# Optimization experiments

Measured on AMD Instinct MI355X. Metric: run time of the kernel, lower is better.

Reference implementation:

```python
import jax, jax.numpy as jnp
import numpy as np

VOCAB, EMB, HID, LAT = 32000, 512, 1024, 512
B, T = 32, 128


def setup_inputs() -> dict:
    key = jax.random.key(0)
    ks = jax.random.split(key, 10)
    s = 0.02
    return {
        "latent_vector": jax.random.normal(ks[0], (B, LAT), jnp.float32),
        "target_tokens": jax.random.randint(ks[1], (B, T), 0, VOCAB),
        "emb": jax.random.normal(ks[2], (VOCAB, EMB), jnp.float32) * s,
        "W_lh": jax.random.normal(ks[3], (HID, LAT), jnp.float32) * s,
        "b_lh": jnp.zeros((HID,), jnp.float32),
        "W_ih": jax.random.normal(ks[4], (4 * HID, EMB), jnp.float32) * s,
        "b_ih": jnp.zeros((4 * HID,), jnp.float32),
        "W_hh": jax.random.normal(ks[5], (4 * HID, HID), jnp.float32) * s,
        "b_hh": jnp.zeros((4 * HID,), jnp.float32),
        "W_out": jax.random.normal(ks[6], (VOCAB, HID), jnp.float32) * s,
        "b_out": jnp.zeros((VOCAB,), jnp.float32),
    }


def reference(latent_vector, target_tokens, emb, W_lh, b_lh, W_ih, b_ih, W_hh, b_hh, W_out, b_out):
    # teacher_forcing_ratio = 1.0 (deterministic): input at step t is target_tokens[:, t-1]
    h = latent_vector @ W_lh.T + b_lh            # [B, HID]
    c = jnp.zeros_like(h)
    xs = emb[target_tokens[:, :-1]]              # [B, T-1, EMB]
    xs = jnp.swapaxes(xs, 0, 1)                  # [T-1, B, EMB]

    def step(carry, x):
        h, c = carry
        gates = x @ W_ih.T + b_ih + h @ W_hh.T + b_hh   # [B, 4*HID]
        i, f, g, o = jnp.split(gates, 4, axis=-1)       # PyTorch LSTM gate order
        c = jax.nn.sigmoid(f) * c + jax.nn.sigmoid(i) * jnp.tanh(g)
        h = jax.nn.sigmoid(o) * jnp.tanh(c)
        logits = h @ W_out.T + b_out                    # [B, VOCAB]
        return (h, c), logits

    _, logits = jax.lax.scan(step, (h, c), xs)          # [T-1, B, VOCAB]
    return jnp.swapaxes(logits, 0, 1)                   # [B, T-1, VOCAB]
```

## Files before the change

kernel.cpp:

```cpp
#include <hip/hip_runtime.h>
#include <cstdint>

typedef __bf16 bf16x8 __attribute__((ext_vector_type(8)));
typedef __bf16 bf16x4 __attribute__((ext_vector_type(4)));
typedef float  f32x4  __attribute__((ext_vector_type(4)));

#define VOCAB 32000
#define EMB   512
#define HID   1024
#define LAT   512
#define BATCH 32
#define TSTEP 127
#define MROWS 4064
#define MPAD  4096
#define G4    4096
#define NBLK  128
#define FSTRIDE 64

__device__ __forceinline__ float sigf(float x){ return 1.0f / (1.0f + __expf(-x)); }
__device__ __forceinline__ float tanhfast(float x){
    float ax = fabsf(x);
    float e  = __expf(-2.0f * ax);
    float t  = (1.0f - e) / (1.0f + e);
    return copysignf(t, x);
}

__device__ __forceinline__ void gll16(void* lds, const void* gsrc){
    __builtin_amdgcn_global_load_lds(
        (const __attribute__((address_space(1))) unsigned int*)gsrc,
        (__attribute__((address_space(3))) unsigned int*)lds,
        16, 0, 0);
}

__global__ __launch_bounds__(256) void cvt_kernel(
    const float* __restrict__ in, __bf16* __restrict__ out, int n4)
{
    int i = blockIdx.x * 256 + threadIdx.x;
    if (i < n4){
        float4 v = ((const float4*)in)[i];
        bf16x4 o = { (__bf16)v.x, (__bf16)v.y, (__bf16)v.z, (__bf16)v.w };
        ((bf16x4*)out)[i] = o;
    }
}

__global__ __launch_bounds__(256) void init_kernel(
    const float* __restrict__ latent,
    const float* __restrict__ Wlh,
    const float* __restrict__ blh,
    __bf16* __restrict__ h0,
    __bf16* __restrict__ Hall,
    unsigned* __restrict__ flags)
{
    if (blockIdx.x == 0 && threadIdx.x < NBLK)
        flags[threadIdx.x * FSTRIDE] = 0u;

    int id = blockIdx.x * 256 + threadIdx.x;
    int b = id >> 10, j = id & 1023;
    float s = blh[j];
    const float4* lr = (const float4*)(latent + (size_t)b * LAT);
    const float4* wr = (const float4*)(Wlh + (size_t)j * LAT);
    for (int k = 0; k < LAT / 4; ++k){
        float4 a = lr[k], w = wr[k];
        s += a.x * w.x + a.y * w.y + a.z * w.z + a.w * w.w;
    }
    h0[id] = (__bf16)s;
    Hall[(size_t)MROWS * HID + id] = (__bf16)0.0f;
}

__global__ __launch_bounds__(256) void gemm_xg(
    const float* __restrict__ emb,
    const float* __restrict__ Wih,
    const int*   __restrict__ tok,
    float*       __restrict__ xg,
    const float* __restrict__ bih,
    const float* __restrict__ bhh)
{
    __shared__ __bf16 As[2][128 * 32];
    __shared__ __bf16 Bs[2][128 * 32];

    const int tid  = threadIdx.x;
    const int wid  = tid >> 6, lane = tid & 63;
    const int tile_n = blockIdx.x, tile_m = blockIdx.y;
    const int wr = wid >> 1, wc = wid & 1;

    f32x4 acc[4][4] = {};

    auto stage = [&](int kt, int buf){
        #pragma unroll
        for (int j = 0; j < 2; ++j){
            const int slot = tid + j * 256;
            const int row  = slot >> 2;
            const int kb   = kt * 32 + (slot & 3) * 8;
            {
                const int brow = tile_n * 128 + row;
                const float4* p = (const float4*)(Wih + (size_t)brow * EMB + kb);
                float4 u = p[0], v = p[1];
                bf16x8 w = { (__bf16)u.x, (__bf16)u.y, (__bf16)u.z, (__bf16)u.w,
                             (__bf16)v.x, (__bf16)v.y, (__bf16)v.z, (__bf16)v.w };
                *(bf16x8*)&Bs[buf][row * 32 + (slot & 3) * 8] = w;
            }
            {
                int r = tile_m * 128 + row;
                int rc = (r < MROWS) ? r : (MROWS - 1);
                int token = tok[(rc & 31) * 128 + (rc >> 5)];
                const float4* p = (const float4*)(emb + (size_t)token * EMB + kb);
                float4 u = p[0], v = p[1];
                bf16x8 w = { (__bf16)u.x, (__bf16)u.y, (__bf16)u.z, (__bf16)u.w,
                             (__bf16)v.x, (__bf16)v.y, (__bf16)v.z, (__bf16)v.w };
                *(bf16x8*)&As[buf][row * 32 + (slot & 3) * 8] = w;
            }
        }
    };

    const int KT = EMB / 32;
    stage(0, 0);
    for (int kt = 0; kt < KT; ++kt){
        const int buf = kt & 1;
        __syncthreads();
        if (kt + 1 < KT) stage(kt + 1, buf ^ 1);
        const __bf16* Abuf = As[buf];
        const __bf16* Bbuf = Bs[buf];
        const int ar = lane & 15, ko = (lane >> 4) * 8;
        bf16x8 av[4], bv[4];
        #pragma unroll
        for (int m = 0; m < 4; ++m)
            av[m] = *(const bf16x8*)&Abuf[(wr * 64 + m * 16 + ar) * 32 + ko];
        #pragma unroll
        for (int n = 0; n < 4; ++n)
            bv[n] = *(const bf16x8*)&Bbuf[(wc * 64 + n * 16 + ar) * 32 + ko];
        #pragma unroll
        for (int m = 0; m < 4; ++m)
            #pragma unroll
            for (int n = 0; n < 4; ++n)
                acc[m][n] = __builtin_amdgcn_mfma_f32_16x16x32_bf16(av[m], bv[n], acc[m][n], 0, 0, 0);
    }

    const int r0 = tile_m * 128 + wr * 64 + ((lane >> 4) << 2);
    const int c0 = tile_n * 128 + wc * 64 + (lane & 15);
    #pragma unroll
    for (int m = 0; m < 4; ++m){
        #pragma unroll
        for (int n = 0; n < 4; ++n){
            const int col = c0 + n * 16;
            float badd = bih[col] + bhh[col];
            #pragma unroll
            for (int q = 0; q < 4; ++q){
                int row = r0 + m * 16 + q;
                xg[(size_t)row * G4 + col] = acc[m][n][q] + badd;
            }
        }
    }
}

#define NTM 32
#define NTN 250
template<int BF16B>
__global__ __launch_bounds__(256) void gemm_logits(
    const __bf16* __restrict__ A,
    const float*  __restrict__ Bf,
    const __bf16* __restrict__ Bb,
    float*        __restrict__ C,
    const float*  __restrict__ bias)
{
    __shared__ __bf16 As[2][128 * 32];
    __shared__ __bf16 Bs[2][128 * 32];

    const int tid  = threadIdx.x;
    const int wid  = tid >> 6, lane = tid & 63;

    const int bid = blockIdx.x;
    const int s   = (bid & 7) * (NTM * NTN / 8) + (bid >> 3);
    const int g   = s / (8 * NTN), rem = s % (8 * NTN);
    const int tile_m = g * 8 + (rem & 7);
    const int tile_n = rem >> 3;

    const int wr = wid >> 1, wc = wid & 1;

    f32x4 acc[4][4] = {};

    auto stage = [&](int kt, int buf){
        const int kb = kt * 32 + (lane & 3) * 8;
        #pragma unroll
        for (int c2 = 0; c2 < 2; ++c2){
            int rA = tile_m * 128 + c2 * 64 + wid * 16 + (lane >> 2);
            gll16(&As[buf][c2 * 2048 + wid * 512], A + (size_t)rA * HID + kb);
            if constexpr (BF16B){
                int rB = tile_n * 128 + c2 * 64 + wid * 16 + (lane >> 2);
                gll16(&Bs[buf][c2 * 2048 + wid * 512], Bb + (size_t)rB * HID + kb);
            }
        }
        if constexpr (!BF16B){
            #pragma unroll
            for (int j = 0; j < 2; ++j){
                const int slot = tid + j * 256;
                const int row  = slot >> 2;
                const int kb2  = kt * 32 + (slot & 3) * 8;
                const int brow = tile_n * 128 + row;
                const float4* p = (const float4*)(Bf + (size_t)brow * HID + kb2);
                float4 u = p[0], v = p[1];
                bf16x8 w = { (__bf16)u.x, (__bf16)u.y, (__bf16)u.z, (__bf16)u.w,
                             (__bf16)v.x, (__bf16)v.y, (__bf16)v.z, (__bf16)v.w };
                *(bf16x8*)&Bs[buf][row * 32 + (slot & 3) * 8] = w;
            }
        }
    };

    const int KT = HID / 32;
    stage(0, 0);
    for (int kt = 0; kt < KT; ++kt){
        const int buf = kt & 1;
        __syncthreads();
        if (kt + 1 < KT) stage(kt + 1, buf ^ 1);
        const __bf16* Abuf = As[buf];
        const __bf16* Bbuf = Bs[buf];
        const int ar = lane & 15, ko = (lane >> 4) * 8;
        bf16x8 av[4], bv[4];
        #pragma unroll
        for (int m = 0; m < 4; ++m)
            av[m] = *(const bf16x8*)&Abuf[(wr * 64 + m * 16 + ar) * 32 + ko];
        #pragma unroll
        for (int n = 0; n < 4; ++n)
            bv[n] = *(const bf16x8*)&Bbuf[(wc * 64 + n * 16 + ar) * 32 + ko];
        #pragma unroll
        for (int m = 0; m < 4; ++m)
            #pragma unroll
            for (int n = 0; n < 4; ++n)
                acc[m][n] = __builtin_amdgcn_mfma_f32_16x16x32_bf16(av[m], bv[n], acc[m][n], 0, 0, 0);
    }

    const int r0 = tile_m * 128 + wr * 64 + ((lane >> 4) << 2);
    const int c0 = tile_n * 128 + wc * 64 + (lane & 15);
    #pragma unroll
    for (int m = 0; m < 4; ++m){
        #pragma unroll
        for (int n = 0; n < 4; ++n){
            const int col = c0 + n * 16;
            float badd = bias[col];
            #pragma unroll
            for (int q = 0; q < 4; ++q){
                int row = r0 + m * 16 + q;
                if (row < MROWS){
                    int t = row >> 5, b = row & 31;
                    __builtin_nontemporal_store(acc[m][n][q] + badd,
                        &C[((size_t)b * TSTEP + t) * VOCAB + col]);
                }
            }
        }
    }
}

__global__ __launch_bounds__(256) void lstm_coop(
    const float*  __restrict__ xg,
    __bf16*       __restrict__ Hall,
    __bf16*       __restrict__ hbuf,
    const __bf16* __restrict__ Whhb,
    unsigned*     __restrict__ flags,
    const float*  __restrict__ Woutf,
    __bf16*       __restrict__ Woutb)
{
    if (blockIdx.x >= NBLK){
        if (Woutb){
            const int n4 = VOCAB * HID / 4;
            int i = (blockIdx.x - NBLK) * 256 + threadIdx.x;
            for (; i < n4; i += NBLK * 256){
                float4 v = ((const float4*)Woutf)[i];
                bf16x4 o = { (__bf16)v.x, (__bf16)v.y, (__bf16)v.z, (__bf16)v.w };
                ((bf16x4*)Woutb)[i] = o;
            }
        }
        return;
    }

    __shared__ float lds_g[4 * 4 * 4 * 64];
    const int tid = threadIdx.x, wid = tid >> 6, lane = tid & 63;
    const int jb = blockIdx.x * 8;

    bf16x8 bfrag[2][8];
    {
        const int gl = lane & 15, ko = (lane >> 4) * 8;
        #pragma unroll
        for (int nt = 0; nt < 2; ++nt){
            int gg = nt * 16 + gl;
            const __bf16* base =
                Whhb + (size_t)((gg >> 3) * HID + jb + (gg & 7)) * HID + wid * 256 + ko;
            #pragma unroll
            for (int ks = 0; ks < 8; ++ks)
                bfrag[nt][ks] = *(const bf16x8*)(base + ks * 32);
        }
    }

    const int b2 = tid >> 2, up0 = (tid & 3) * 2;
    const int mt2 = b2 >> 4, r2 = b2 & 15, reg2 = r2 & 3, lb2 = (r2 >> 2) << 4;
    float cst[2] = {0.0f, 0.0f};

    const float* xq = xg + (size_t)b2 * G4 + jb + up0;
    float2 xv[4];
    if (tid < 128){
        #pragma unroll
        for (int g = 0; g < 4; ++g) xv[g] = *(const float2*)(xq + g * HID);
    }

    const size_t e0 = (size_t)(lane & 15) * HID + wid * 256 + (lane >> 4) * 8;

    for (int t = 0; t < TSTEP; ++t){
        unsigned long long* hq = (unsigned long long*)(hbuf + (size_t)(t & 1) * (BATCH * HID));
        union { unsigned long long q[2]; bf16x8 v; } xa[16];
        #pragma unroll
        for (int ks = 0; ks < 8; ++ks){
            size_t q0 = (e0 + (size_t)ks * 32) >> 2;
            size_t q1 = q0 + ((size_t)16 * HID >> 2);
            xa[ks].q[0]     = __hip_atomic_load(hq + q0,     __ATOMIC_RELAXED, __HIP_MEMORY_SCOPE_AGENT);
            xa[ks].q[1]     = __hip_atomic_load(hq + q0 + 1, __ATOMIC_RELAXED, __HIP_MEMORY_SCOPE_AGENT);
            xa[8 + ks].q[0] = __hip_atomic_load(hq + q1,     __ATOMIC_RELAXED, __HIP_MEMORY_SCOPE_AGENT);
            xa[8 + ks].q[1] = __hip_atomic_load(hq + q1 + 1, __ATOMIC_RELAXED, __HIP_MEMORY_SCOPE_AGENT);
        }
        f32x4 a00 = {}, a01 = {}, a10 = {}, a11 = {};
        #pragma unroll
        for (int ks = 0; ks < 8; ++ks){
            a00 = __builtin_amdgcn_mfma_f32_16x16x32_bf16(xa[ks].v,     bfrag[0][ks], a00, 0, 0, 0);
            a01 = __builtin_amdgcn_mfma_f32_16x16x32_bf16(xa[ks].v,     bfrag[1][ks], a01, 0, 0, 0);
            a10 = __builtin_amdgcn_mfma_f32_16x16x32_bf16(xa[8 + ks].v, bfrag[0][ks], a10, 0, 0, 0);
            a11 = __builtin_amdgcn_mfma_f32_16x16x32_bf16(xa[8 + ks].v, bfrag[1][ks], a11, 0, 0, 0);
        }
        #pragma unroll
        for (int q = 0; q < 4; ++q){
            lds_g[((0 * 4 + wid) * 4 + q) * 64 + lane] = a00[q];
            lds_g[((1 * 4 + wid) * 4 + q) * 64 + lane] = a01[q];
            lds_g[((2 * 4 + wid) * 4 + q) * 64 + lane] = a10[q];
            lds_g[((3 * 4 + wid) * 4 + q) * 64 + lane] = a11[q];
        }
        __syncthreads();

        if (tid < 128){
            const float* xn = xq + (size_t)(t + 1) * (BATCH * G4);
            float2 xnew[4];
            #pragma unroll
            for (int g = 0; g < 4; ++g) xnew[g] = *(const float2*)(xn + g * HID);

            float h2[2];
            #pragma unroll
            for (int du = 0; du < 2; ++du){
                int u2 = up0 + du;
                float gate[4];
                #pragma unroll
                for (int ty = 0; ty < 4; ++ty){
                    int gg = ty * 8 + u2;
                    int mtnt = mt2 * 2 + (gg >> 4);
                    int li = lb2 | (gg & 15);
                    float s = 0.0f;
                    #pragma unroll
                    for (int w = 0; w < 4; ++w)
                        s += lds_g[((mtnt * 4 + w) * 4 + reg2) * 64 + li];
                    gate[ty] = s;
                }
                float gi = gate[0] + ((du == 0) ? xv[0].x : xv[0].y);
                float gf = gate[1] + ((du == 0) ? xv[1].x : xv[1].y);
                float gc = gate[2] + ((du == 0) ? xv[2].x : xv[2].y);
                float go = gate[3] + ((du == 0) ? xv[3].x : xv[3].y);
                float c = sigf(gf) * cst[du] + sigf(gi) * tanhfast(gc);
                cst[du] = c;
                h2[du] = sigf(go) * tanhfast(c);
            }
            #pragma unroll
            for (int g = 0; g < 4; ++g) xv[g] = xnew[g];

            union { __bf16 h[2]; unsigned u; } pk;
            pk.h[0] = (__bf16)h2[0]; pk.h[1] = (__bf16)h2[1];
            unsigned* hw = (unsigned*)(hbuf + (size_t)((t + 1) & 1) * (BATCH * HID)
                                       + (size_t)b2 * HID + jb + up0);
            __hip_atomic_store(hw, pk.u, __ATOMIC_RELAXED, __HIP_MEMORY_SCOPE_AGENT);
            *(unsigned*)(Hall + ((size_t)t * BATCH + b2) * HID + jb + up0) = pk.u;
        }

        if (t + 1 == TSTEP) break;

        __syncthreads();
        if (wid == 0){
            if (lane == 0){
                __hip_atomic_store(&flags[blockIdx.x * FSTRIDE], (unsigned)(t + 1),
                                   __ATOMIC_RELAXED, __HIP_MEMORY_SCOPE_AGENT);
            }
            const unsigned tgt = (unsigned)(t + 1);
            for (;;){
                unsigned f0 = __hip_atomic_load(&flags[lane * FSTRIDE],
                                  __ATOMIC_RELAXED, __HIP_MEMORY_SCOPE_AGENT);
                unsigned f1 = __hip_atomic_load(&flags[(lane + 64) * FSTRIDE],
                                  __ATOMIC_RELAXED, __HIP_MEMORY_SCOPE_AGENT);
                if (f0 >= tgt && f1 >= tgt) break;
                __builtin_amdgcn_s_sleep(1);
            }
        }
        __syncthreads();
    }
}

extern "C" void kernel_launch(void* const* d_in, const int* in_sizes, int n_in,
                              void* d_out, int out_size, void* d_ws, size_t ws_size,
                              hipStream_t stream)
{
    const float* latent = (const float*)d_in[0];
    const int*   tokens = (const int*)d_in[1];
    const float* emb    = (const float*)d_in[2];
    const float* Wlh    = (const float*)d_in[3];
    const float* blh    = (const float*)d_in[4];
    const float* Wih    = (const float*)d_in[5];
    const float* bih    = (const float*)d_in[6];
    const float* Whh    = (const float*)d_in[7];
    const float* bhh    = (const float*)d_in[8];
    const float* Wout   = (const float*)d_in[9];
    const float* bout   = (const float*)d_in[10];
    float* out = (float*)d_out;

    const size_t xg_b   = (size_t)MPAD * G4 * 4;
    const size_t hall_b = (size_t)MPAD * HID * 2;
    const size_t whh_b  = (size_t)G4 * HID * 2;
    const size_t wout_b = (size_t)VOCAB * HID * 2;
    const size_t hb_b   = (size_t)2 * BATCH * HID * 2;
    const size_t cnt_b  = (size_t)NBLK * FSTRIDE * 4;

    char* p = (char*)d_ws;
    const bool wsA = ws_size >= xg_b + hall_b + whh_b + wout_b + hb_b + cnt_b;
    const bool wsB = ws_size >= hall_b + whh_b + wout_b + hb_b + cnt_b;

    float* xg;
    if (wsA){ xg = (float*)p; p += xg_b; }
    else    { xg = (float*)d_out; }
    __bf16* Hall = (__bf16*)p; p += hall_b;
    __bf16* Whhb = (__bf16*)p; p += whh_b;
    __bf16* Woutb = nullptr;
    if (wsA || wsB){ Woutb = (__bf16*)p; p += wout_b; }
    __bf16* hbuf = (__bf16*)p; p += hb_b;
    unsigned* flags = (unsigned*)p; p += cnt_b;

    cvt_kernel<<<dim3(G4 * HID / 4 / 256), dim3(256), 0, stream>>>(
        Whh, Whhb, G4 * HID / 4);

    init_kernel<<<dim3(128), dim3(256), 0, stream>>>(latent, Wlh, blh, hbuf, Hall, flags);

    gemm_xg<<<dim3(G4 / 128, MPAD / 128), dim3(256), 0, stream>>>(
        emb, Wih, tokens, xg, bih, bhh);

    {
        const float*  xgc   = xg;
        __bf16*       hallp = Hall;
        __bf16*       hbp   = hbuf;
        const __bf16* whhp  = Whhb;
        unsigned*     flagp = flags;
        const float*  wof   = Wout;
        __bf16*       wob   = Woutb;
        void* args[] = { (void*)&xgc, (void*)&hallp, (void*)&hbp, (void*)&whhp,
                         (void*)&flagp, (void*)&wof, (void*)&wob };
        hipLaunchCooperativeKernel((void*)lstm_coop, dim3(2 * NBLK), dim3(256), args, 0, stream);
    }

    if (Woutb)
        gemm_logits<1><<<dim3(NTM * NTN), dim3(256), 0, stream>>>(
            Hall, (const float*)nullptr, Woutb, out, bout);
    else
        gemm_logits<0><<<dim3(NTM * NTN), dim3(256), 0, stream>>>(
            Hall, Wout, (const __bf16*)nullptr, out, bout);
}
```

Baseline: 1.219 ms.

## Overlap output-projection GEMM with LSTM recurrence in one cooperative mega-kernel

Fuses the LSTM recurrence and the vocab logits GEMM into one cooperative launch. 128 blocks run the recurrence, and 768 extra blocks compute logits tiles as soon as a global done-counter shows the required timesteps of H are written. The Whh and Wout bf16 conversions move into the init and xg-GEMM kernels, and the flags are packed contiguously so one 64-bit load checks two blocks. The aim is to hide the large output GEMM behind the latency-bound serial recurrence. The risks are contention from the GEMM blocks slowing the critical recurrence path (mitigated with setprio), and a co-residency requirement of 896 blocks that could fail and fall back.

```diff
diff --git a/kernel.cpp b/kernel.cpp
--- a/kernel.cpp
+++ b/kernel.cpp
@@ -15,7 +15,9 @@
 #define MPAD  4096
 #define G4    4096
 #define NBLK  128
-#define FSTRIDE 64
+#define NG    768
+#define NTM   32
+#define NTN   250
 
 __device__ __forceinline__ float sigf(float x){ return 1.0f / (1.0f + __expf(-x)); }
 __device__ __forceinline__ float tanhfast(float x){
@@ -32,27 +34,26 @@
         16, 0, 0);
 }
 
-__global__ __launch_bounds__(256) void cvt_kernel(
-    const float* __restrict__ in, __bf16* __restrict__ out, int n4)
-{
-    int i = blockIdx.x * 256 + threadIdx.x;
-    if (i < n4){
-        float4 v = ((const float4*)in)[i];
-        bf16x4 o = { (__bf16)v.x, (__bf16)v.y, (__bf16)v.z, (__bf16)v.w };
-        ((bf16x4*)out)[i] = o;
-    }
-}
-
 __global__ __launch_bounds__(256) void init_kernel(
     const float* __restrict__ latent,
     const float* __restrict__ Wlh,
     const float* __restrict__ blh,
     __bf16* __restrict__ h0,
     __bf16* __restrict__ Hall,
-    unsigned* __restrict__ flags)
+    unsigned* __restrict__ flags,
+    const float* __restrict__ Whh,
+    __bf16* __restrict__ Whhb)
 {
-    if (blockIdx.x == 0 && threadIdx.x < NBLK)
-        flags[threadIdx.x * FSTRIDE] = 0u;
+    if (blockIdx.x >= 128){
+        const int n4 = G4 * HID / 4;
+        for (int i = (blockIdx.x - 128) * 256 + threadIdx.x; i < n4; i += 64 * 256){
+            float4 v = ((const float4*)Whh)[i];
+            bf16x4 o = { (__bf16)v.x, (__bf16)v.y, (__bf16)v.z, (__bf16)v.w };
+            ((bf16x4*)Whhb)[i] = o;
+        }
+        return;
+    }
+    if (blockIdx.x == 0) flags[threadIdx.x] = 0u;
 
     int id = blockIdx.x * 256 + threadIdx.x;
     int b = id >> 10, j = id & 1023;
@@ -73,8 +74,23 @@
     const int*   __restrict__ tok,
     float*       __restrict__ xg,
     const float* __restrict__ bih,
-    const float* __restrict__ bhh)
+    const float* __restrict__ bhh,
+    const float* __restrict__ Woutf,
+    __bf16*      __restrict__ Woutb)
 {
+    if (blockIdx.y >= MPAD / 128){
+        if (Woutb){
+            const int n4 = VOCAB * HID / 4;
+            int cb = (blockIdx.y - 32) * 32 + blockIdx.x;
+            for (int i = cb * 256 + threadIdx.x; i < n4; i += 256 * 256){
+                float4 v = ((const float4*)Woutf)[i];
+                bf16x4 o = { (__bf16)v.x, (__bf16)v.y, (__bf16)v.z, (__bf16)v.w };
+                ((bf16x4*)Woutb)[i] = o;
+            }
+        }
+        return;
+    }
+
     __shared__ __bf16 As[2][128 * 32];
     __shared__ __bf16 Bs[2][128 * 32];
 
@@ -152,8 +168,6 @@
     }
 }
 
-#define NTM 32
-#define NTN 250
 template<int BF16B>
 __global__ __launch_bounds__(256) void gemm_logits(
     const __bf16* __restrict__ A,
@@ -167,13 +181,11 @@
 
     const int tid  = threadIdx.x;
     const int wid  = tid >> 6, lane = tid & 63;
-
     const int bid = blockIdx.x;
     const int s   = (bid & 7) * (NTM * NTN / 8) + (bid >> 3);
     const int g   = s / (8 * NTN), rem = s % (8 * NTN);
     const int tile_m = g * 8 + (rem & 7);
     const int tile_n = rem >> 3;
-
     const int wr = wid >> 1, wc = wid & 1;
 
     f32x4 acc[4][4] = {};
@@ -249,145 +261,222 @@
     }
 }
 
-__global__ __launch_bounds__(256) void lstm_coop(
+__global__ __launch_bounds__(256, 4) void mega_kernel(
     const float*  __restrict__ xg,
     __bf16*       __restrict__ Hall,
     __bf16*       __restrict__ hbuf,
     const __bf16* __restrict__ Whhb,
     unsigned*     __restrict__ flags,
-    const float*  __restrict__ Woutf,
-    __bf16*       __restrict__ Woutb)
+    const __bf16* __restrict__ Woutb,
+    float*        __restrict__ C,
+    const float*  __restrict__ bout)
 {
-    if (blockIdx.x >= NBLK){
-        if (Woutb){
-            const int n4 = VOCAB * HID / 4;
-            int i = (blockIdx.x - NBLK) * 256 + threadIdx.x;
-            for (; i < n4; i += NBLK * 256){
-                float4 v = ((const float4*)Woutf)[i];
-                bf16x4 o = { (__bf16)v.x, (__bf16)v.y, (__bf16)v.z, (__bf16)v.w };
-                ((bf16x4*)Woutb)[i] = o;
-            }
+    __shared__ __align__(16) char smem[32768];
+    unsigned* done = flags + 160;
+
+    if (blockIdx.x < NBLK){
+        __builtin_amdgcn_s_setprio(3);
+        float* lds_g = (float*)smem;
+        const int tid = threadIdx.x, wid = tid >> 6, lane = tid & 63;
+        const int jb = blockIdx.x * 8;
+
+        bf16x8 bfrag[2][8];
+        {
+            const int gl = lane & 15, ko = (lane >> 4) * 8;
+            #pragma unroll
+            for (int nt = 0; nt < 2; ++nt){
+                int gg = nt * 16 + gl;
+                const __bf16* base =
+                    Whhb + (size_t)((gg >> 3) * HID + jb + (gg & 7)) * HID + wid * 256 + ko;
+                #pragma unroll
+                for (int ks = 0; ks < 8; ++ks)
+                    bfrag[nt][ks] = *(const bf16x8*)(base + ks * 32);
+            }
+        }
+
+        const int b2 = tid >> 2, up0 = (tid & 3) * 2;
+        const int mt2 = b2 >> 4, r2 = b2 & 15, reg2 = r2 & 3, lb2 = (r2 >> 2) << 4;
+        float cst[2] = {0.0f, 0.0f};
+
+        const float* xq = xg + (size_t)b2 * G4 + jb + up0;
+        float2 xv[4];
+        if (tid < 128){
+            #pragma unroll
+            for (int g = 0; g < 4; ++g) xv[g] = *(const float2*)(xq + g * HID);
+        }
+
+        const size_t e0 = (size_t)(lane & 15) * HID + wid * 256 + (lane >> 4) * 8;
+
+        for (int t = 0; t < TSTEP; ++t){
+            unsigned long long* hq = (unsigned long long*)(hbuf + (size_t)(t & 1) * (BATCH * HID));
+            union { unsigned long long q[2]; bf16x8 v; } xa[16];
+            #pragma unroll
+            for (int ks = 0; ks < 8; ++ks){
+                size_t q0 = (e0 + (size_t)ks * 32) >> 2;
+                size_t q1 = q0 + ((size_t)16 * HID >> 2);
+                xa[ks].q[0]     = __hip_atomic_load(hq + q0,     __ATOMIC_RELAXED, __HIP_MEMORY_SCOPE_AGENT);
+                xa[ks].q[1]     = __hip_atomic_load(hq + q0 + 1, __ATOMIC_RELAXED, __HIP_MEMORY_SCOPE_AGENT);
+                xa[8 + ks].q[0] = __hip_atomic_load(hq + q1,     __ATOMIC_RELAXED, __HIP_MEMORY_SCOPE_AGENT);
+                xa[8 + ks].q[1] = __hip_atomic_load(hq + q1 + 1, __ATOMIC_RELAXED, __HIP_MEMORY_SCOPE_AGENT);
+            }
+            f32x4 a00 = {}, a01 = {}, a10 = {}, a11 = {};
+            #pragma unroll
+            for (int ks = 0; ks < 8; ++ks){
+                a00 = __builtin_amdgcn_mfma_f32_16x16x32_bf16(xa[ks].v,     bfrag[0][ks], a00, 0, 0, 0);
+                a01 = __builtin_amdgcn_mfma_f32_16x16x32_bf16(xa[ks].v,     bfrag[1][ks], a01, 0, 0, 0);
+                a10 = __builtin_amdgcn_mfma_f32_16x16x32_bf16(xa[8 + ks].v, bfrag[0][ks], a10, 0, 0, 0);
+                a11 = __builtin_amdgcn_mfma_f32_16x16x32_bf16(xa[8 + ks].v, bfrag[1][ks], a11, 0, 0, 0);
+            }
+            #pragma unroll
+            for (int q = 0; q < 4; ++q){
+                lds_g[((0 * 4 + wid) * 4 + q) * 64 + lane] = a00[q];
+                lds_g[((1 * 4 + wid) * 4 + q) * 64 + lane] = a01[q];
+                lds_g[((2 * 4 + wid) * 4 + q) * 64 + lane] = a10[q];
+                lds_g[((3 * 4 + wid) * 4 + q) * 64 + lane] = a11[q];
+            }
+            __syncthreads();
+
+            if (tid < 128){
+                const float* xn = xq + (size_t)(t + 1) * (BATCH * G4);
+                float2 xnew[4];
+                #pragma unroll
+                for (int g = 0; g < 4; ++g) xnew[g] = *(const float2*)(xn + g * HID);
+
+                float h2[2];
+                #pragma unroll
+                for (int du = 0; du < 2; ++du){
+                    int u2 = up0 + du;
+                    float gate[4];
+                    #pragma unroll
+                    for (int ty = 0; ty < 4; ++ty){
+                        int gg = ty * 8 + u2;
+                        int mtnt = mt2 * 2 + (gg >> 4);
+                        int li = lb2 | (gg & 15);
+                        float s = 0.0f;
+                        #pragma unroll
+                        for (int w = 0; w < 4; ++w)
+                            s += lds_g[((mtnt * 4 + w) * 4 + reg2) * 64 + li];
+                        gate[ty] = s;
+                    }
+                    float gi = gate[0] + ((du == 0) ? xv[0].x : xv[0].y);
+                    float gf = gate[1] + ((du == 0) ? xv[1].x : xv[1].y);
+                    float gc = gate[2] + ((du == 0) ? xv[2].x : xv[2].y);
+                    float go = gate[3] + ((du == 0) ? xv[3].x : xv[3].y);
+                    float c = sigf(gf) * cst[du] + sigf(gi) * tanhfast(gc);
+                    cst[du] = c;
+                    h2[du] = sigf(go) * tanhfast(c);
+                }
+                #pragma unroll
+                for (int g = 0; g < 4; ++g) xv[g] = xnew[g];
+
+                union { __bf16 h[2]; unsigned u; } pk;
+                pk.h[0] = (__bf16)h2[0]; pk.h[1] = (__bf16)h2[1];
+                unsigned* hw = (unsigned*)(hbuf + (size_t)((t + 1) & 1) * (BATCH * HID)
+                                           + (size_t)b2 * HID + jb + up0);
+                __hip_atomic_store(hw, pk.u, __ATOMIC_RELAXED, __HIP_MEMORY_SCOPE_AGENT);
+                __hip_atomic_store((unsigned*)(Hall + ((size_t)t * BATCH + b2) * HID + jb + up0),
+                                   pk.u, __ATOMIC_RELAXED, __HIP_MEMORY_SCOPE_AGENT);
+            }
+
+            __syncthreads();
+            if (wid == 0){
+                if (lane == 0)
+                    __hip_atomic_store(&flags[blockIdx.x], (unsigned)(t + 1),
+                                       __ATOMIC_RELAXED, __HIP_MEMORY_SCOPE_AGENT);
+                const unsigned tgt = (unsigned)(t + 1);
+                if (t + 1 < TSTEP || blockIdx.x == 0){
+                    const unsigned long long* fq = (const unsigned long long*)flags;
+                    for (;;){
+                        unsigned long long v = __hip_atomic_load(&fq[lane],
+                                      __ATOMIC_RELAXED, __HIP_MEMORY_SCOPE_AGENT);
+                        if ((unsigned)v >= tgt && (unsigned)(v >> 32) >= tgt) break;
+                        __builtin_amdgcn_s_sleep(1);
+                    }
+                    if (blockIdx.x == 0 && lane == 0)
+                        __hip_atomic_store(done, tgt, __ATOMIC_RELAXED, __HIP_MEMORY_SCOPE_AGENT);
+                }
+            }
+            __syncthreads();
         }
         return;
     }
 
-    __shared__ float lds_g[4 * 4 * 4 * 64];
-    const int tid = threadIdx.x, wid = tid >> 6, lane = tid & 63;
-    const int jb = blockIdx.x * 8;
-
-    bf16x8 bfrag[2][8];
-    {
-        const int gl = lane & 15, ko = (lane >> 4) * 8;
-        #pragma unroll
-        for (int nt = 0; nt < 2; ++nt){
-            int gg = nt * 16 + gl;
-            const __bf16* base =
-                Whhb + (size_t)((gg >> 3) * HID + jb + (gg & 7)) * HID + wid * 256 + ko;
-            #pragma unroll
-            for (int ks = 0; ks < 8; ++ks)
-                bfrag[nt][ks] = *(const bf16x8*)(base + ks * 32);
-        }
-    }
-
-    const int b2 = tid >> 2, up0 = (tid & 3) * 2;
-    const int mt2 = b2 >> 4, r2 = b2 & 15, reg2 = r2 & 3, lb2 = (r2 >> 2) << 4;
-    float cst[2] = {0.0f, 0.0f};
-
-    const float* xq = xg + (size_t)b2 * G4 + jb + up0;
-    float2 xv[4];
-    if (tid < 128){
-        #pragma unroll
-        for (int g = 0; g < 4; ++g) xv[g] = *(const float2*)(xq + g * HID);
-    }
-
-    const size_t e0 = (size_t)(lane & 15) * HID + wid * 256 + (lane >> 4) * 8;
-
-    for (int t = 0; t < TSTEP; ++t){
-        unsigned long long* hq = (unsigned long long*)(hbuf + (size_t)(t & 1) * (BATCH * HID));
-        union { unsigned long long q[2]; bf16x8 v; } xa[16];
-        #pragma unroll
-        for (int ks = 0; ks < 8; ++ks){
-            size_t q0 = (e0 + (size_t)ks * 32) >> 2;
-            size_t q1 = q0 + ((size_t)16 * HID >> 2);
-            xa[ks].q[0]     = __hip_atomic_load(hq + q0,     __ATOMIC_RELAXED, __HIP_MEMORY_SCOPE_AGENT);
-            xa[ks].q[1]     = __hip_atomic_load(hq + q0 + 1, __ATOMIC_RELAXED, __HIP_MEMORY_SCOPE_AGENT);
-            xa[8 + ks].q[0] = __hip_atomic_load(hq + q1,     __ATOMIC_RELAXED, __HIP_MEMORY_SCOPE_AGENT);
-            xa[8 + ks].q[1] = __hip_atomic_load(hq + q1 + 1, __ATOMIC_RELAXED, __HIP_MEMORY_SCOPE_AGENT);
-        }
-        f32x4 a00 = {}, a01 = {}, a10 = {}, a11 = {};
-        #pragma unroll
-        for (int ks = 0; ks < 8; ++ks){
-            a00 = __builtin_amdgcn_mfma_f32_16x16x32_bf16(xa[ks].v,     bfrag[0][ks], a00, 0, 0, 0);
-            a01 = __builtin_amdgcn_mfma_f32_16x16x32_bf16(xa[ks].v,     bfrag[1][ks], a01, 0, 0, 0);
-            a10 = __builtin_amdgcn_mfma_f32_16x16x32_bf16(xa[8 + ks].v, bfrag[0][ks], a10, 0, 0, 0);
-            a11 = __builtin_amdgcn_mfma_f32_16x16x32_bf16(xa[8 + ks].v, bfrag[1][ks], a11, 0, 0, 0);
-        }
-        #pragma unroll
-        for (int q = 0; q < 4; ++q){
-            lds_g[((0 * 4 + wid) * 4 + q) * 64 + lane] = a00[q];
-            lds_g[((1 * 4 + wid) * 4 + q) * 64 + lane] = a01[q];
-            lds_g[((2 * 4 + wid) * 4 + q) * 64 + lane] = a10[q];
-            lds_g[((3 * 4 + wid) * 4 + q) * 64 + lane] = a11[q];
-        }
-        __syncthreads();
-
-        if (tid < 128){
-            const float* xn = xq + (size_t)(t + 1) * (BATCH * G4);
-            float2 xnew[4];
-            #pragma unroll
-            for (int g = 0; g < 4; ++g) xnew[g] = *(const float2*)(xn + g * HID);
-
-            float h2[2];
-            #pragma unroll
-            for (int du = 0; du < 2; ++du){
-                int u2 = up0 + du;
-                float gate[4];
+    if (!Woutb) return;
+    __bf16* As0 = (__bf16*)smem;
+    __bf16* Bs0 = (__bf16*)(smem + 16384);
+
+    const int gid = blockIdx.x - NBLK;
+    const int tid = threadIdx.x;
+    const int wid = tid >> 6, lane = tid & 63;
+    const int wr = wid >> 1, wc = wid & 1;
+    unsigned seen = 0;
+
+    for (int i = gid; i < NTM * NTN; i += NG){
+        const int tm = i / NTN, tn = i - tm * NTN;
+        const unsigned need = (unsigned)((tm * 4 + 4 > TSTEP) ? TSTEP : tm * 4 + 4);
+        if (seen < need){
+            for (;;){
+                unsigned d = __hip_atomic_load(done, __ATOMIC_RELAXED, __HIP_MEMORY_SCOPE_AGENT);
+                if (d >= need){ seen = d; break; }
+                __builtin_amdgcn_s_sleep(32);
+            }
+        }
+
+        f32x4 acc[4][4] = {};
+
+        auto stage = [&](int kt, int buf){
+            __bf16* Ad = As0 + buf * 4096;
+            __bf16* Bd = Bs0 + buf * 4096;
+            const int kb = kt * 32 + (lane & 3) * 8;
+            #pragma unroll
+            for (int c2 = 0; c2 < 2; ++c2){
+                int rA = tm * 128 + c2 * 64 + wid * 16 + (lane >> 2);
+                gll16(Ad + c2 * 2048 + wid * 512, Hall + (size_t)rA * HID + kb);
+                int rB = tn * 128 + c2 * 64 + wid * 16 + (lane >> 2);
+                gll16(Bd + c2 * 2048 + wid * 512, Woutb + (size_t)rB * HID + kb);
+            }
+        };
+
+        const int KT = HID / 32;
+        stage(0, 0);
+        for (int kt = 0; kt < KT; ++kt){
+            const int buf = kt & 1;
+            __syncthreads();
+            if (kt + 1 < KT) stage(kt + 1, buf ^ 1);
+            const __bf16* Abuf = As0 + buf * 4096;
+            const __bf16* Bbuf = Bs0 + buf * 4096;
+            const int ar = lane & 15, ko = (lane >> 4) * 8;
+            bf16x8 av[4], bv[4];
+            #pragma unroll
+            for (int m = 0; m < 4; ++m)
+                av[m] = *(const bf16x8*)&Abuf[(wr * 64 + m * 16 + ar) * 32 + ko];
+            #pragma unroll
+            for (int n = 0; n < 4; ++n)
+                bv[n] = *(const bf16x8*)&Bbuf[(wc * 64 + n * 16 + ar) * 32 + ko];
+            #pragma unroll
+            for (int m = 0; m < 4; ++m)
                 #pragma unroll
-                for (int ty = 0; ty < 4; ++ty){
-                    int gg = ty * 8 + u2;
-                    int mtnt = mt2 * 2 + (gg >> 4);
-                    int li = lb2 | (gg & 15);
-                    float s = 0.0f;
-                    #pragma unroll
-                    for (int w = 0; w < 4; ++w)
-                        s += lds_g[((mtnt * 4 + w) * 4 + reg2) * 64 + li];
-                    gate[ty] = s;
+                for (int n = 0; n < 4; ++n)
+                    acc[m][n] = __builtin_amdgcn_mfma_f32_16x16x32_bf16(av[m], bv[n], acc[m][n], 0, 0, 0);
+        }
+
+        const int r0 = tm * 128 + wr * 64 + ((lane >> 4) << 2);
+        const int c0 = tn * 128 + wc * 64 + (lane & 15);
+        #pragma unroll
+        for (int m = 0; m < 4; ++m){
+            #pragma unroll
+            for (int n = 0; n < 4; ++n){
+                const int col = c0 + n * 16;
+                float badd = bout[col];
+                #pragma unroll
+                for (int q = 0; q < 4; ++q){
+                    int row = r0 + m * 16 + q;
+                    if (row < MROWS){
+                        int t = row >> 5, b = row & 31;
+                        __builtin_nontemporal_store(acc[m][n][q] + badd,
+                            &C[((size_t)b * TSTEP + t) * VOCAB + col]);
+                    }
                 }
-                float gi = gate[0] + ((du == 0) ? xv[0].x : xv[0].y);
-                float gf = gate[1] + ((du == 0) ? xv[1].x : xv[1].y);
-                float gc = gate[2] + ((du == 0) ? xv[2].x : xv[2].y);
-                float go = gate[3] + ((du == 0) ? xv[3].x : xv[3].y);
-                float c = sigf(gf) * cst[du] + sigf(gi) * tanhfast(gc);
-                cst[du] = c;
-                h2[du] = sigf(go) * tanhfast(c);
-            }
-            #pragma unroll
-            for (int g = 0; g < 4; ++g) xv[g] = xnew[g];
-
-            union { __bf16 h[2]; unsigned u; } pk;
-            pk.h[0] = (__bf16)h2[0]; pk.h[1] = (__bf16)h2[1];
-            unsigned* hw = (unsigned*)(hbuf + (size_t)((t + 1) & 1) * (BATCH * HID)
-                                       + (size_t)b2 * HID + jb + up0);
-            __hip_atomic_store(hw, pk.u, __ATOMIC_RELAXED, __HIP_MEMORY_SCOPE_AGENT);
-            *(unsigned*)(Hall + ((size_t)t * BATCH + b2) * HID + jb + up0) = pk.u;
-        }
-
-        if (t + 1 == TSTEP) break;
-
-        __syncthreads();
-        if (wid == 0){
-            if (lane == 0){
-                __hip_atomic_store(&flags[blockIdx.x * FSTRIDE], (unsigned)(t + 1),
-                                   __ATOMIC_RELAXED, __HIP_MEMORY_SCOPE_AGENT);
-            }
-            const unsigned tgt = (unsigned)(t + 1);
-            for (;;){
-                unsigned f0 = __hip_atomic_load(&flags[lane * FSTRIDE],
-                                  __ATOMIC_RELAXED, __HIP_MEMORY_SCOPE_AGENT);
-                unsigned f1 = __hip_atomic_load(&flags[(lane + 64) * FSTRIDE],
-                                  __ATOMIC_RELAXED, __HIP_MEMORY_SCOPE_AGENT);
-                if (f0 >= tgt && f1 >= tgt) break;
-                __builtin_amdgcn_s_sleep(1);
             }
         }
         __syncthreads();
@@ -416,7 +505,7 @@
     const size_t whh_b  = (size_t)G4 * HID * 2;
     const size_t wout_b = (size_t)VOCAB * HID * 2;
     const size_t hb_b   = (size_t)2 * BATCH * HID * 2;
-    const size_t cnt_b  = (size_t)NBLK * FSTRIDE * 4;
+    const size_t cnt_b  = 1024;
 
     char* p = (char*)d_ws;
     const bool wsA = ws_size >= xg_b + hall_b + whh_b + wout_b + hb_b + cnt_b;
@@ -432,31 +521,40 @@
     __bf16* hbuf = (__bf16*)p; p += hb_b;
     unsigned* flags = (unsigned*)p; p += cnt_b;
 
-    cvt_kernel<<<dim3(G4 * HID / 4 / 256), dim3(256), 0, stream>>>(
-        Whh, Whhb, G4 * HID / 4);
-
-    init_kernel<<<dim3(128), dim3(256), 0, stream>>>(latent, Wlh, blh, hbuf, Hall, flags);
-
-    gemm_xg<<<dim3(G4 / 128, MPAD / 128), dim3(256), 0, stream>>>(
-        emb, Wih, tokens, xg, bih, bhh);
-
-    {
-        const float*  xgc   = xg;
-        __bf16*       hallp = Hall;
-        __bf16*       hbp   = hbuf;
-        const __bf16* whhp  = Whhb;
-        unsigned*     flagp = flags;
-        const float*  wof   = Wout;
-        __bf16*       wob   = Woutb;
-        void* args[] = { (void*)&xgc, (void*)&hallp, (void*)&hbp, (void*)&whhp,
-                         (void*)&flagp, (void*)&wof, (void*)&wob };
-        hipLaunchCooperativeKernel((void*)lstm_coop, dim3(2 * NBLK), dim3(256), args, 0, stream);
-    }
-
-    if (Woutb)
-        gemm_logits<1><<<dim3(NTM * NTN), dim3(256), 0, stream>>>(
-            Hall, (const float*)nullptr, Woutb, out, bout);
-    else
-        gemm_logits<0><<<dim3(NTM * NTN), dim3(256), 0, stream>>>(
-            Hall, Wout, (const __bf16*)nullptr, out, bout);
-}
+    init_kernel<<<dim3(192), dim3(256), 0, stream>>>(
+        latent, Wlh, blh, hbuf, Hall, flags, Whh, Whhb);
+
+    gemm_xg<<<dim3(G4 / 128, MPAD / 128 + 8), dim3(256), 0, stream>>>(
+        emb, Wih, tokens, xg, bih, bhh, Wout, Woutb);
+
+    const __bf16* wob_mega = wsA ? Woutb : nullptr;
+    const float*  xgc   = xg;
+    __bf16*       hallp = Hall;
+    __bf16*       hbp   = hbuf;
+    const __bf16* whhp  = Whhb;
+    unsigned*     flagp = flags;
+    float*        outp  = out;
+    const float*  boutp = bout;
+    void* args[] = { (void*)&xgc, (void*)&hallp, (void*)&hbp, (void*)&whhp,
+                     (void*)&flagp, (void*)&wob_mega, (void*)&outp, (void*)&boutp };
+    hipError_t cerr = hipLaunchCooperativeKernel(
+        (void*)mega_kernel, dim3(wsA ? NBLK + NG : NBLK), dim3(256), args, 0, stream);
+
+    bool mega_gemm = wsA && (cerr == hipSuccess);
+    if (cerr != hipSuccess){
+        const __bf16* wob_null = nullptr;
+        void* args2[] = { (void*)&xgc, (void*)&hallp, (void*)&hbp, (void*)&whhp,
+                          (void*)&flagp, (void*)&wob_null, (void*)&outp, (void*)&boutp };
+        hipLaunchCooperativeKernel((void*)mega_kernel, dim3(NBLK), dim3(256),
+                                   args2, 0, stream);
+    }
+
+    if (!mega_gemm){
+        if (Woutb)
+            gemm_logits<1><<<dim3(NTM * NTN), dim3(256), 0, stream>>>(
+                Hall, (const float*)nullptr, Woutb, out, bout);
+        else
+            gemm_logits<0><<<dim3(NTM * NTN), dim3(256), 0, stream>>>(
+                Hall, Wout, (const __bf16*)nullptr, out, bout);
+    }
+}
```

Result: slower. 1.579 ms (+29.5%).

## Pack LSTM step flags densely, read h from Hall, fuse Whh conversion into init

Applied to the files above, without the earlier changes.

Replaces the padded per-block flag array with densely packed flags, so each lane polls two block flags with one 64-bit load. The separate double-buffered h buffer is dropped: each step reads the previous hidden state straight from Hall, which removes one store per step. The Whh fp32-to-bf16 conversion is folded into the init kernel, saving one launch. Dense flags put all blocks' flags on shared cache lines, which may add contention while blocks write them.

```diff
diff --git a/kernel.cpp b/kernel.cpp
--- a/kernel.cpp
+++ b/kernel.cpp
@@ -15,7 +15,8 @@
 #define MPAD  4096
 #define G4    4096
 #define NBLK  128
-#define FSTRIDE 64
+#define NTM   32
+#define NTN   250
 
 __device__ __forceinline__ float sigf(float x){ return 1.0f / (1.0f + __expf(-x)); }
 __device__ __forceinline__ float tanhfast(float x){
@@ -32,27 +33,26 @@
         16, 0, 0);
 }
 
-__global__ __launch_bounds__(256) void cvt_kernel(
-    const float* __restrict__ in, __bf16* __restrict__ out, int n4)
-{
-    int i = blockIdx.x * 256 + threadIdx.x;
-    if (i < n4){
-        float4 v = ((const float4*)in)[i];
-        bf16x4 o = { (__bf16)v.x, (__bf16)v.y, (__bf16)v.z, (__bf16)v.w };
-        ((bf16x4*)out)[i] = o;
-    }
-}
-
 __global__ __launch_bounds__(256) void init_kernel(
     const float* __restrict__ latent,
     const float* __restrict__ Wlh,
     const float* __restrict__ blh,
     __bf16* __restrict__ h0,
     __bf16* __restrict__ Hall,
-    unsigned* __restrict__ flags)
+    unsigned* __restrict__ flags,
+    const float* __restrict__ Whh,
+    __bf16* __restrict__ Whhb)
 {
-    if (blockIdx.x == 0 && threadIdx.x < NBLK)
-        flags[threadIdx.x * FSTRIDE] = 0u;
+    if (blockIdx.x >= 128){
+        const int n4 = G4 * HID / 4;
+        for (int i = (blockIdx.x - 128) * 256 + threadIdx.x; i < n4; i += 64 * 256){
+            float4 v = ((const float4*)Whh)[i];
+            bf16x4 o = { (__bf16)v.x, (__bf16)v.y, (__bf16)v.z, (__bf16)v.w };
+            ((bf16x4*)Whhb)[i] = o;
+        }
+        return;
+    }
+    if (blockIdx.x == 0) flags[threadIdx.x] = 0u;
 
     int id = blockIdx.x * 256 + threadIdx.x;
     int b = id >> 10, j = id & 1023;
@@ -152,8 +152,6 @@
     }
 }
 
-#define NTM 32
-#define NTN 250
 template<int BF16B>
 __global__ __launch_bounds__(256) void gemm_logits(
     const __bf16* __restrict__ A,
@@ -167,13 +165,11 @@
 
     const int tid  = threadIdx.x;
     const int wid  = tid >> 6, lane = tid & 63;
-
     const int bid = blockIdx.x;
     const int s   = (bid & 7) * (NTM * NTN / 8) + (bid >> 3);
     const int g   = s / (8 * NTN), rem = s % (8 * NTN);
     const int tile_m = g * 8 + (rem & 7);
     const int tile_n = rem >> 3;
-
     const int wr = wid >> 1, wc = wid & 1;
 
     f32x4 acc[4][4] = {};
@@ -252,7 +248,7 @@
 __global__ __launch_bounds__(256) void lstm_coop(
     const float*  __restrict__ xg,
     __bf16*       __restrict__ Hall,
-    __bf16*       __restrict__ hbuf,
+    const __bf16* __restrict__ h0,
     const __bf16* __restrict__ Whhb,
     unsigned*     __restrict__ flags,
     const float*  __restrict__ Woutf,
@@ -261,8 +257,7 @@
     if (blockIdx.x >= NBLK){
         if (Woutb){
             const int n4 = VOCAB * HID / 4;
-            int i = (blockIdx.x - NBLK) * 256 + threadIdx.x;
-            for (; i < n4; i += NBLK * 256){
+            for (int i = (blockIdx.x - NBLK) * 256 + threadIdx.x; i < n4; i += NBLK * 256){
                 float4 v = ((const float4*)Woutf)[i];
                 bf16x4 o = { (__bf16)v.x, (__bf16)v.y, (__bf16)v.z, (__bf16)v.w };
                 ((bf16x4*)Woutb)[i] = o;
@@ -303,7 +298,8 @@
     const size_t e0 = (size_t)(lane & 15) * HID + wid * 256 + (lane >> 4) * 8;
 
     for (int t = 0; t < TSTEP; ++t){
-        unsigned long long* hq = (unsigned long long*)(hbuf + (size_t)(t & 1) * (BATCH * HID));
+        const __bf16* hsrc = (t == 0) ? h0 : (Hall + (size_t)(t - 1) * (BATCH * HID));
+        const unsigned long long* hq = (const unsigned long long*)hsrc;
         union { unsigned long long q[2]; bf16x8 v; } xa[16];
         #pragma unroll
         for (int ks = 0; ks < 8; ++ks){
@@ -366,10 +362,8 @@
 
             union { __bf16 h[2]; unsigned u; } pk;
             pk.h[0] = (__bf16)h2[0]; pk.h[1] = (__bf16)h2[1];
-            unsigned* hw = (unsigned*)(hbuf + (size_t)((t + 1) & 1) * (BATCH * HID)
-                                       + (size_t)b2 * HID + jb + up0);
-            __hip_atomic_store(hw, pk.u, __ATOMIC_RELAXED, __HIP_MEMORY_SCOPE_AGENT);
-            *(unsigned*)(Hall + ((size_t)t * BATCH + b2) * HID + jb + up0) = pk.u;
+            __hip_atomic_store((unsigned*)(Hall + ((size_t)t * BATCH + b2) * HID + jb + up0),
+                               pk.u, __ATOMIC_RELAXED, __HIP_MEMORY_SCOPE_AGENT);
         }
 
         if (t + 1 == TSTEP) break;
@@ -377,16 +371,15 @@
         __syncthreads();
         if (wid == 0){
             if (lane == 0){
-                __hip_atomic_store(&flags[blockIdx.x * FSTRIDE], (unsigned)(t + 1),
+                __hip_atomic_store(&flags[blockIdx.x], (unsigned)(t + 1),
                                    __ATOMIC_RELAXED, __HIP_MEMORY_SCOPE_AGENT);
             }
             const unsigned tgt = (unsigned)(t + 1);
+            const unsigned long long* fq = (const unsigned long long*)flags;
             for (;;){
-                unsigned f0 = __hip_atomic_load(&flags[lane * FSTRIDE],
-                                  __ATOMIC_RELAXED, __HIP_MEMORY_SCOPE_AGENT);
-                unsigned f1 = __hip_atomic_load(&flags[(lane + 64) * FSTRIDE],
-                                  __ATOMIC_RELAXED, __HIP_MEMORY_SCOPE_AGENT);
-                if (f0 >= tgt && f1 >= tgt) break;
+                unsigned long long v = __hip_atomic_load(&fq[lane],
+                              __ATOMIC_RELAXED, __HIP_MEMORY_SCOPE_AGENT);
+                if ((unsigned)v >= tgt && (unsigned)(v >> 32) >= tgt) break;
                 __builtin_amdgcn_s_sleep(1);
             }
         }
@@ -415,12 +408,12 @@
     const size_t hall_b = (size_t)MPAD * HID * 2;
     const size_t whh_b  = (size_t)G4 * HID * 2;
     const size_t wout_b = (size_t)VOCAB * HID * 2;
-    const size_t hb_b   = (size_t)2 * BATCH * HID * 2;
-    const size_t cnt_b  = (size_t)NBLK * FSTRIDE * 4;
+    const size_t h0_b   = (size_t)BATCH * HID * 2;
+    const size_t cnt_b  = 1024;
 
     char* p = (char*)d_ws;
-    const bool wsA = ws_size >= xg_b + hall_b + whh_b + wout_b + hb_b + cnt_b;
-    const bool wsB = ws_size >= hall_b + whh_b + wout_b + hb_b + cnt_b;
+    const bool wsA = ws_size >= xg_b + hall_b + whh_b + wout_b + h0_b + cnt_b;
+    const bool wsB = ws_size >= hall_b + whh_b + wout_b + h0_b + cnt_b;
 
     float* xg;
     if (wsA){ xg = (float*)p; p += xg_b; }
@@ -429,13 +422,11 @@
     __bf16* Whhb = (__bf16*)p; p += whh_b;
     __bf16* Woutb = nullptr;
     if (wsA || wsB){ Woutb = (__bf16*)p; p += wout_b; }
-    __bf16* hbuf = (__bf16*)p; p += hb_b;
+    __bf16* h0 = (__bf16*)p; p += h0_b;
     unsigned* flags = (unsigned*)p; p += cnt_b;
 
-    cvt_kernel<<<dim3(G4 * HID / 4 / 256), dim3(256), 0, stream>>>(
-        Whh, Whhb, G4 * HID / 4);
-
-    init_kernel<<<dim3(128), dim3(256), 0, stream>>>(latent, Wlh, blh, hbuf, Hall, flags);
+    init_kernel<<<dim3(192), dim3(256), 0, stream>>>(
+        latent, Wlh, blh, h0, Hall, flags, Whh, Whhb);
 
     gemm_xg<<<dim3(G4 / 128, MPAD / 128), dim3(256), 0, stream>>>(
         emb, Wih, tokens, xg, bih, bhh);
@@ -443,14 +434,15 @@
     {
         const float*  xgc   = xg;
         __bf16*       hallp = Hall;
-        __bf16*       hbp   = hbuf;
+        const __bf16* h0p   = h0;
         const __bf16* whhp  = Whhb;
         unsigned*     flagp = flags;
         const float*  wof   = Wout;
         __bf16*       wob   = Woutb;
-        void* args[] = { (void*)&xgc, (void*)&hallp, (void*)&hbp, (void*)&whhp,
+        void* args[] = { (void*)&xgc, (void*)&hallp, (void*)&h0p, (void*)&whhp,
                          (void*)&flagp, (void*)&wof, (void*)&wob };
-        hipLaunchCooperativeKernel((void*)lstm_coop, dim3(2 * NBLK), dim3(256), args, 0, stream);
+        hipLaunchCooperativeKernel((void*)lstm_coop, dim3(2 * NBLK), dim3(256),
+                                   args, 0, stream);
     }
 
     if (Woutb)
```

Measured after the change: 1.522 ms. 24.8% more time.
